# Performance work log

Measured on AMD Instinct MI355X. Metric: run time of the kernel, lower is better.

Reference implementation:

```python
import jax, jax.numpy as jnp
import numpy as np

B, C, H, W = 16, 384, 64, 64
S, R, GR = 16, 8, 64
EPS = 1e-6


def setup_inputs() -> dict:
    key = jax.random.key(0)
    ks = jax.random.split(key, 16)
    def rn(k, shape, s):
        return jax.random.normal(k, shape, dtype=jnp.float32) * s
    inp = {"x": jax.random.normal(ks[0], (B, C, H, W), dtype=jnp.float32)}
    i = 1
    for p in ("row", "col"):
        inp[p + "_a_logit"] = jnp.zeros((S,), jnp.float32)
        inp[p + "_U"] = rn(ks[i], (S, R), 0.02); i += 1
        inp[p + "_V"] = rn(ks[i], (S, R), 0.02); i += 1
        inp[p + "_Win"] = rn(ks[i], (S, C), 1.0 / np.sqrt(C)); i += 1
        inp[p + "_bin"] = jnp.zeros((S,), jnp.float32)
        inp[p + "_Wg"] = rn(ks[i], (S, C), 1.0 / np.sqrt(C)); i += 1
        inp[p + "_bg"] = jnp.zeros((S,), jnp.float32)
        inp[p + "_Wout"] = rn(ks[i], (C, S), 1.0 / np.sqrt(S)); i += 1
        inp[p + "_bout"] = jnp.zeros((C,), jnp.float32)
        inp[p + "_Wskip"] = rn(ks[i], (C, C), 1.0 / np.sqrt(C)); i += 1
        inp[p + "_bskip"] = jnp.zeros((C,), jnp.float32)
    inp["g1_w"] = rn(ks[i], (GR, C), 1.0 / np.sqrt(C)); i += 1
    inp["g1_b"] = jnp.zeros((GR,), jnp.float32)
    inp["g2_w"] = rn(ks[i], (C, GR), 1.0 / np.sqrt(GR)); i += 1
    inp["g2_b"] = jnp.zeros((C,), jnp.float32)
    inp["norm_w"] = jnp.ones((C,), jnp.float32)
    inp["norm_b"] = jnpp = jnp.zeros((C,), jnp.float32)
    inp["norm_b"] = jnp.zeros((C,), jnp.float32)
    return inp


def _ssm1d(x, a_logit, U, V, Win, bin_, Wg, bg, Wout, bout, Wskip, bskip, reverse):
    # x: [N, L, D]
    if reverse:
        x = x[:, ::-1]
    u = jnp.einsum('nld,sd->nls', x, Win) + bin_          # [N,L,S]
    g = jax.nn.sigmoid(jnp.einsum('nld,sd->nls', x, Wg) + bg)
    a = jax.nn.sigmoid(a_logit)                            # [S]
    # h_t = a*h + g_t*u_t + h @ (U V^T)^T  ==  h @ (diag(a) + (U V^T)^T) + g_t*u_t
    A = jnp.diag(a) + (U @ V.T).T                          # [S,S]
    gu = jnp.swapaxes(g * u, 0, 1)                         # [L,N,S]
    h0 = jnp.zeros((x.shape[0], a.shape[0]), x.dtype)

    def step(h, gu_t):
        h = h @ A + gu_t
        return h, h

    _, hs = jax.lax.scan(step, h0, gu)                     # [L,N,S]
    hs = jnp.swapaxes(hs, 0, 1)                            # [N,L,S]
    y = (jnp.einsum('nls,ds->nld', hs, Wout) + bout
         + jnp.einsum('nld,ed->nle', x, Wskip) + bskip)
    if reverse:
        y = y[:, ::-1]
    return y


def _forward(x, rp, cp, g1_w, g1_b, g2_w, g2_b, norm_w, norm_b):
    Bx, Cx, Hx, Wx = x.shape
    rows = jnp.transpose(x, (0, 2, 3, 1)).reshape(Bx * Hx, Wx, Cx)
    cols = jnp.transpose(x, (0, 3, 2, 1)).reshape(Bx * Wx, Hx, Cx)
    yr = _ssm1d(rows, *rp, False) + _ssm1d(rows, *rp, True)
    yc = _ssm1d(cols, *cp, False) + _ssm1d(cols, *cp, True)
    yr = jnp.transpose(yr.reshape(Bx, Hx, Wx, Cx), (0, 3, 1, 2))
    yc = jnp.transpose(yc.reshape(Bx, Wx, Hx, Cx), (0, 3, 2, 1))
    y = (yr + yc) * 0.25
    # LayerNorm over channel dim of BCHW
    mean = x.mean(axis=1, keepdims=True)
    var = ((x - mean) ** 2).mean(axis=1, keepdims=True)
    xn = (x - mean) / jnp.sqrt(var + EPS)
    xn = xn * norm_w[None, :, None, None] + norm_b[None, :, None, None]
    # gate: 1x1 conv -> GELU(exact) -> 1x1 conv -> sigmoid
    h1 = jax.nn.gelu(jnp.einsum('bchw,oc->bohw', xn, g1_w) + g1_b[None, :, None, None], approximate=False)
    g = jax.nn.sigmoid(jnp.einsum('bghw,cg->bchw', h1, g2_w) + g2_b[None, :, None, None])
    return g * y + (1.0 - g) * x


def reference(x, row_a_logit, row_U, row_V, row_Win, row_bin, row_Wg, row_bg, row_Wout, row_bout, row_Wskip, row_bskip, col_a_logit, col_U, col_V, col_Win, col_bin, col_Wg, col_bg, col_Wout, col_bout, col_Wskip, col_bskip, g1_w, g1_b, g2_w, g2_b, norm_w, norm_b):
    rp = (row_a_logit, row_U, row_V, row_Win, row_bin, row_Wg, row_bg, row_Wout, row_bout, row_Wskip, row_bskip)
    cp = (col_a_logit, col_U, col_V, col_Win, col_bin, col_Wg, col_bg, col_Wout, col_bout, col_Wskip, col_bskip)
    return _forward(x, rp, cp, g1_w, g1_b, g2_w, g2_b, norm_w, norm_b)
```

## Files before the change

### kernel.cpp

```cpp
#include <hip/hip_runtime.h>
#include <hip/hip_bf16.h>
#include <math.h>

#define PP 4096
#define CCH 384
#define NB 16

using short8 = __attribute__((ext_vector_type(8))) short;
using f32x4  = __attribute__((ext_vector_type(4))) float;
using half2t = __attribute__((ext_vector_type(2))) __fp16;

__device__ __forceinline__ float sigmoidf_(float v){ return 1.f/(1.f+expf(-v)); }
__device__ __forceinline__ float fast_sig(float v){
  return __builtin_amdgcn_rcpf(1.f + __builtin_amdgcn_exp2f(-v*1.44269504088896f));
}
__device__ __forceinline__ unsigned int f2bf(float f){
  __hip_bfloat16 h = __float2bfloat16(f);
  return (unsigned int)*reinterpret_cast<unsigned short*>(&h);
}
__device__ __forceinline__ float bf2f(unsigned short u){
  unsigned int w = ((unsigned int)u) << 16;
  return __uint_as_float(w);
}
__device__ __forceinline__ void gload_lds16(const void* g, void* l){
  __builtin_amdgcn_global_load_lds(
      (const __attribute__((address_space(1))) unsigned int*)g,
      (__attribute__((address_space(3))) unsigned int*)l, 16, 0, 0);
}

__global__ __launch_bounds__(256) void k_prep(
    const float* __restrict__ rAl, const float* __restrict__ rU, const float* __restrict__ rV,
    const float* __restrict__ cAl, const float* __restrict__ cU, const float* __restrict__ cV,
    const float* __restrict__ rWs, const float* __restrict__ cWs,
    const float* __restrict__ WinR, const float* __restrict__ WgR,
    const float* __restrict__ WinC, const float* __restrict__ WgC,
    const float* __restrict__ g1w, const float* __restrict__ nw, const float* __restrict__ nb,
    const float* __restrict__ g2w,
    const float* __restrict__ WoR, const float* __restrict__ WoC,
    float* __restrict__ Arow, float* __restrict__ Acol,
    unsigned short* __restrict__ WsumBf, unsigned short* __restrict__ WcatBf,
    unsigned short* __restrict__ g2wBf, unsigned short* __restrict__ WocatBf,
    float* __restrict__ t1, float* __restrict__ t2)
{
  int bid = blockIdx.x, tid = threadIdx.x;
  if (bid < 576) {
    int idx = bid*256 + tid;
    WsumBf[idx] = (unsigned short)f2bf(rWs[idx] + cWs[idx]);
  } else if (bid < 768) {
    int idx = (bid-576)*256 + tid;
    int row = idx / CCH, col = idx - row*CCH;
    float v;
    if      (row < 16)  v = WinR[row*CCH + col];
    else if (row < 32)  v = WgR [(row-16)*CCH + col];
    else if (row < 48)  v = WinC[(row-32)*CCH + col];
    else if (row < 64)  v = WgC [(row-48)*CCH + col];
    else                v = g1w[(row-64)*CCH + col]*nw[col];
    WcatBf[idx] = (unsigned short)f2bf(v);
  } else if (bid < 864) {
    int idx = (bid-768)*256 + tid;
    g2wBf[idx] = (unsigned short)f2bf(g2w[idx]);
  } else if (bid < 960) {
    int idx = (bid-864)*256 + tid;
    int c = idx >> 6, k = idx & 63;
    int sel = (k >> 4) & 1;
    float v = 0.5f * (sel ? WoC[c*16 + (k&15)] : WoR[c*16 + (k&15)]);
    WocatBf[idx] = (unsigned short)f2bf(v);
  } else {
    {
      int i = tid >> 4, j = tid & 15;
      float sr = 0.f, sc = 0.f;
      #pragma unroll
      for (int r=0;r<8;++r){ sr += rV[i*8+r]*rU[j*8+r]; sc += cV[i*8+r]*cU[j*8+r]; }
      if (i==j){ sr += sigmoidf_(rAl[i]); sc += sigmoidf_(cAl[i]); }
      Arow[tid] = sr; Acol[tid] = sc;
    }
    if (tid < 64) {
      float s1=0.f, s2=0.f;
      for (int c=0;c<CCH;++c){ s1 += g1w[tid*CCH+c]*nw[c]; s2 += nb[c]*g1w[tid*CCH+c]; }
      t1[tid]=s1; t2[tid]=s2;
    }
  }
}

__global__ __launch_bounds__(256) void k_xf(
    const float* __restrict__ x, const unsigned short* __restrict__ WcatBf,
    const float* __restrict__ binR, const float* __restrict__ bgR,
    const float* __restrict__ binC, const float* __restrict__ bgC,
    const float* __restrict__ t1, const float* __restrict__ t2,
    const float* __restrict__ g1b,
    unsigned short* __restrict__ xbf,
    float* __restrict__ ugr, float* __restrict__ ugc,
    unsigned short* __restrict__ h1bf)
{
  int b = blockIdx.x >> 6, pt = blockIdx.x & 63;
  int t = threadIdx.x;
  int w = t >> 6, l = t & 63;
  int lr = l & 15, kq = l >> 4, kb8 = kq*8;
  int pl = t & 63, g4 = w;

  __shared__ unsigned short xtb[64*64];
  __shared__ float red[512];
  __shared__ float meanS[64], invS[64];

  const float* xb = x + (size_t)b*CCH*PP + pt*64;
  f32x4 acc[2][4] = {};
  float sx = 0.f, sx2 = 0.f;

  float xv[16];
  #pragma unroll
  for (int j=0;j<16;++j) xv[j] = xb[(size_t)(g4*16 + j)*PP + pl];

  const unsigned short* wrow0 = WcatBf + (size_t)(w*32 + lr)*CCH + kb8;
  const unsigned short* wrow1 = wrow0 + 16*CCH;
  unsigned short* xgo = xbf + ((size_t)(b*PP + pt*64))*CCH;

  #pragma unroll
  for (int cc=0; cc<6; ++cc) {
    unsigned int pk[8];
    #pragma unroll
    for (int j=0;j<16;++j){ sx += xv[j]; sx2 += xv[j]*xv[j]; }
    #pragma unroll
    for (int j=0;j<8;++j) pk[j] = f2bf(xv[2*j]) | (f2bf(xv[2*j+1])<<16);
    __syncthreads();
    {
      int kg0 = g4*2, kg1 = g4*2+1;
      uint4 v0 = make_uint4(pk[0],pk[1],pk[2],pk[3]);
      uint4 v1 = make_uint4(pk[4],pk[5],pk[6],pk[7]);
      *(uint4*)&xtb[(size_t)(pl*8 + (kg0 ^ (pl&7)))*8] = v0;
      *(uint4*)&xtb[(size_t)(pl*8 + (kg1 ^ (pl&7)))*8] = v1;
    }
    if (cc < 5) {
      #pragma unroll
      for (int j=0;j<16;++j) xv[j] = xb[(size_t)((cc+1)*64 + g4*16 + j)*PP + pl];
    }
    short8 a0k0 = *(const short8*)(wrow0 + cc*64);
    short8 a0k1 = *(const short8*)(wrow0 + cc*64 + 32);
    short8 a1k0 = *(const short8*)(wrow1 + cc*64);
    short8 a1k1 = *(const short8*)(wrow1 + cc*64 + 32);
    __syncthreads();
    #pragma unroll
    for (int ks=0; ks<2; ++ks){
      int kg = ks*4 + kq;
      #pragma unroll
      for (int nf=0; nf<4; ++nf){
        int pr = nf*16 + lr;
        short8 bv = *(const short8*)&xtb[(size_t)(pr*8 + (kg ^ (pr&7)))*8];
        acc[0][nf] = __builtin_amdgcn_mfma_f32_16x16x32_bf16(ks? a0k1:a0k0, bv, acc[0][nf], 0,0,0);
        acc[1][nf] = __builtin_amdgcn_mfma_f32_16x16x32_bf16(ks? a1k1:a1k0, bv, acc[1][nf], 0,0,0);
      }
    }
    #pragma unroll
    for (int it=0; it<2; ++it){
      int p2 = 32*it + (t>>3), kg2 = t & 7;
      uint4 v = *(const uint4*)&xtb[(size_t)(p2*8 + (kg2 ^ (p2&7)))*8];
      *(uint4*)&xgo[(size_t)p2*CCH + cc*64 + kg2*8] = v;
    }
  }

  __syncthreads();
  red[g4*64 + pl] = sx;
  red[256 + g4*64 + pl] = sx2;
  __syncthreads();
  if (t < 64) {
    float s1 = red[t] + red[64+t] + red[128+t] + red[192+t];
    float s2 = red[256+t] + red[320+t] + red[384+t] + red[448+t];
    float mu = s1 * (1.f/CCH);
    float var = s2 * (1.f/CCH) - mu*mu;
    meanS[t] = mu;
    invS[t]  = rsqrtf(var + 1e-6f);
  }
  __syncthreads();

  if (w < 2) {
    const float* bu = w ? binC : binR;
    const float* bg = w ? bgC  : bgR;
    float* dst = w ? ugc : ugr;
    float bus[4], bgs[4];
    #pragma unroll
    for (int r=0;r<4;++r){ int s = kq*4 + r; bus[r]=bu[s]; bgs[r]=bg[s]; }
    #pragma unroll
    for (int nf=0; nf<4; ++nf){
      size_t pbase = ((size_t)(b*PP + pt*64 + nf*16 + lr))*16;
      #pragma unroll
      for (int r=0;r<4;++r){
        int s = kq*4 + r;
        float u = acc[0][nf][r] + bus[r];
        float g = fast_sig(acc[1][nf][r] + bgs[r]);
        dst[pbase + s] = u*g;
      }
    }
  } else {
    int ob = (w-2)*32 + kq*4;
    float t1o[2][4], t2o[2][4], gbo[2][4];
    #pragma unroll
    for (int mi=0;mi<2;++mi)
      #pragma unroll
      for (int r=0;r<4;++r){
        int o = ob + mi*16 + r;
        t1o[mi][r]=t1[o]; t2o[mi][r]=t2[o]; gbo[mi][r]=g1b[o];
      }
    #pragma unroll
    for (int nf=0; nf<4; ++nf){
      int pLoc = nf*16 + lr;
      float mu = meanS[pLoc], iv = invS[pLoc];
      #pragma unroll
      for (int mi=0;mi<2;++mi){
        unsigned int us[4];
        #pragma unroll
        for (int r=0;r<4;++r){
          float pre = iv*(acc[mi][nf][r] - mu*t1o[mi][r]) + t2o[mi][r] + gbo[mi][r];
          float ge = 0.5f*pre*(1.f + erff(pre*0.70710678118654752f));
          us[r] = f2bf(ge);
        }
        uint2 o2; o2.x = us[0] | (us[1]<<16); o2.y = us[2] | (us[3]<<16);
        *reinterpret_cast<uint2*>(h1bf + ((size_t)(b*PP + pt*64 + pLoc))*64 + (w-2)*32 + mi*16 + kq*4) = o2;
      }
    }
  }
}

__global__ __launch_bounds__(256) void k_scan(
    const float* __restrict__ ugr, const float* __restrict__ ugc,
    const float* __restrict__ Arow, const float* __restrict__ Acol,
    unsigned short* __restrict__ hs2)
{
  int W = blockIdx.x*4 + (threadIdx.x >> 6);
  int lane = threadIdx.x & 63;
  int tsk = W*4 + (lane >> 4);
  int s = lane & 15, base = lane & 48;
  int dir = tsk >> 11;
  int rem = tsk & 2047;
  int isCol = rem >> 10;
  int gg = rem & 1023;
  int b = gg >> 6, rc = gg & 63;
  const float* ug = isCol ? ugc : ugr;
  const float* A  = isCol ? Acol : Arow;
  int off = dir*32 + isCol*16;
  int p0 = b*PP + (isCol ? rc : rc*64);
  int stride = isCol ? 64 : 1;
  float ac[16];
  #pragma unroll
  for (int i=0;i<16;++i) ac[i] = A[i*16 + s];
  float h = 0.f;
  #pragma unroll 4
  for (int st=0; st<64; ++st){
    int l2 = dir ? (63-st) : st;
    float gu = ug[((size_t)(p0 + l2*stride))*16 + s];
    float tt = 0.f;
    #pragma unroll
    for (int i=0;i<16;++i) tt += __shfl(h, base + i, 64) * ac[i];
    h = tt + gu;
    hs2[((size_t)(p0 + l2*stride))*64 + off + s] = (unsigned short)f2bf(h);
  }
}

__global__ __launch_bounds__(512, 4) void k_fused(
    const unsigned short* __restrict__ xbf,
    const unsigned short* __restrict__ WsumBf,
    const unsigned short* __restrict__ h1bf, const unsigned short* __restrict__ g2wBf,
    const unsigned short* __restrict__ hs2, const unsigned short* __restrict__ WocatBf,
    const float* __restrict__ g2b,
    const float* __restrict__ boR, const float* __restrict__ bsR,
    const float* __restrict__ boC, const float* __restrict__ bsC,
    float* __restrict__ outp)
{
  int obid = blockIdx.x;
  int bid = ((obid & 7) * 128) + (obid >> 3);
  int b = bid >> 6, pt = bid & 63;
  int t = threadIdx.x;
  int w = t >> 6, l = t & 63;
  int lr = l & 15, kq = l >> 4, kb8 = kq * 8;
  int cw = w*48;

  __shared__ unsigned short xt[64*48*8];

  short8 gaw[3][2], gbv[2][4];
  {
    const unsigned short* hbase = h1bf + ((size_t)(b*PP + pt*64 + lr))*64 + kb8;
    #pragma unroll
    for (int ks=0; ks<2; ++ks)
      #pragma unroll
      for (int nf=0; nf<4; ++nf)
        gbv[ks][nf] = *(const short8*)(hbase + (size_t)nf*16*64 + ks*32);
    #pragma unroll
    for (int mi=0; mi<3; ++mi){
      const unsigned short* wbg = g2wBf + (size_t)(cw + mi*16 + lr)*64 + kb8;
      gaw[mi][0] = *(const short8*)(wbg);
      gaw[mi][1] = *(const short8*)(wbg + 32);
    }
  }

  {
    const unsigned short* xrow0 = xbf + ((size_t)(b*PP + pt*64))*CCH;
    #pragma unroll
    for (int i=0;i<6;++i){
      int G = w*384 + i*64 + l;
      int p = G/48, kgs = G - p*48;
      int kg = (kgs & ~7) | ((kgs & 7) ^ (p & 7));
      gload_lds16(xrow0 + (size_t)p*CCH + kg*8, &xt[(size_t)G*8]);
    }
  }

  unsigned int gt[3][4][2];
  {
    f32x4 gac[3][4] = {};
    #pragma unroll
    for (int ks=0; ks<2; ++ks)
      #pragma unroll
      for (int nf=0; nf<4; ++nf)
        #pragma unroll
        for (int mi=0; mi<3; ++mi)
          gac[mi][nf] = __builtin_amdgcn_mfma_f32_16x16x32_bf16(gaw[mi][ks], gbv[ks][nf], gac[mi][nf], 0,0,0);
    #pragma unroll
    for (int mi=0;mi<3;++mi){
      float4 gb4 = *(const float4*)&g2b[cw + mi*16 + kq*4];
      #pragma unroll
      for (int nf=0;nf<4;++nf){
        float s0 = fast_sig(gac[mi][nf][0] + gb4.x);
        float s1 = fast_sig(gac[mi][nf][1] + gb4.y);
        float s2 = fast_sig(gac[mi][nf][2] + gb4.z);
        float s3 = fast_sig(gac[mi][nf][3] + gb4.w);
        half2t p01 = __builtin_amdgcn_cvt_pkrtz(s0, s1);
        half2t p23 = __builtin_amdgcn_cvt_pkrtz(s2, s3);
        __builtin_memcpy(&gt[mi][nf][0], &p01, 4);
        __builtin_memcpy(&gt[mi][nf][1], &p23, 4);
      }
    }
  }

  __syncthreads();

  f32x4 acc[3][4] = {};
  const unsigned short* wbS = WsumBf + (size_t)(cw + lr)*CCH + kb8;
  #pragma unroll
  for (int c=0;c<6;++c){
    short8 a[3][2];
    #pragma unroll
    for (int mi=0;mi<3;++mi){
      a[mi][0] = *(const short8*)(wbS + (size_t)mi*16*CCH + c*64);
      a[mi][1] = *(const short8*)(wbS + (size_t)mi*16*CCH + c*64 + 32);
    }
    #pragma unroll
    for (int ks=0;ks<2;++ks){
      int kgl = ks*4 + kq;
      #pragma unroll
      for (int nf=0;nf<4;++nf){
        int pr = nf*16 + lr;
        int kgs = c*8 + (kgl ^ (pr & 7));
        short8 bv = *(const short8*)&xt[(size_t)(pr*48 + kgs)*8];
        #pragma unroll
        for (int mi=0;mi<3;++mi)
          acc[mi][nf] = __builtin_amdgcn_mfma_f32_16x16x32_bf16(a[mi][ks], bv, acc[mi][nf], 0,0,0);
      }
    }
  }

  {
    const unsigned short* hb2 = hs2 + ((size_t)(b*PP + pt*64 + lr))*64 + kb8;
    short8 hv[2][4];
    #pragma unroll
    for (int ks=0;ks<2;++ks)
      #pragma unroll
      for (int nf=0;nf<4;++nf)
        hv[ks][nf] = *(const short8*)(hb2 + (size_t)nf*16*64 + ks*32);
    #pragma unroll
    for (int mi=0;mi<3;++mi){
      const unsigned short* wo = WocatBf + (size_t)(cw + mi*16 + lr)*64 + kb8;
      short8 wa0 = *(const short8*)(wo);
      short8 wa1 = *(const short8*)(wo + 32);
      #pragma unroll
      for (int nf=0;nf<4;++nf){
        acc[mi][nf] = __builtin_amdgcn_mfma_f32_16x16x32_bf16(wa0, hv[0][nf], acc[mi][nf], 0,0,0);
        acc[mi][nf] = __builtin_amdgcn_mfma_f32_16x16x32_bf16(wa1, hv[1][nf], acc[mi][nf], 0,0,0);
      }
    }
  }

  #pragma unroll
  for (int mi=0;mi<3;++mi){
    int cb0 = cw + mi*16 + kq*4;
    float4 b1 = *(const float4*)&boR[cb0];
    float4 b2 = *(const float4*)&bsR[cb0];
    float4 b3 = *(const float4*)&boC[cb0];
    float4 b4 = *(const float4*)&bsC[cb0];
    float cb4[4] = { b1.x+b2.x+b3.x+b4.x, b1.y+b2.y+b3.y+b4.y,
                     b1.z+b2.z+b3.z+b4.z, b1.w+b2.w+b3.w+b4.w };
    int kgR = cb0 >> 3, eoff = cb0 & 7;
    #pragma unroll
    for (int nf=0;nf<4;++nf){
      int p = nf*16 + lr;
      int kgsR = (kgR & ~7) | ((kgR & 7) ^ (p & 7));
      uint2 xres = *(const uint2*)&xt[(size_t)(p*48 + kgsR)*8 + eoff];
      half2t g01, g23;
      __builtin_memcpy(&g01, &gt[mi][nf][0], 4);
      __builtin_memcpy(&g23, &gt[mi][nf][1], 4);
      float gv[4] = { (float)g01[0], (float)g01[1], (float)g23[0], (float)g23[1] };
      #pragma unroll
      for (int r=0;r<4;++r){
        unsigned int word = (r < 2) ? xres.x : xres.y;
        unsigned short us = (r & 1) ? (unsigned short)(word >> 16) : (unsigned short)(word & 0xffff);
        float xv = bf2f(us);
        float y = 0.5f*acc[mi][nf][r] + 0.5f*cb4[r];
        float gtv = gv[r];
        size_t addr = ((size_t)(b*CCH + cb0 + r))*PP + pt*64 + p;
        outp[addr] = gtv*y + (1.f-gtv)*xv;
      }
    }
  }
}

extern "C" void kernel_launch(void* const* d_in, const int* in_sizes, int n_in,
                              void* d_out, int out_size, void* d_ws, size_t ws_size,
                              hipStream_t stream)
{
  const float* x    = (const float*)d_in[0];
  const float* rAl  = (const float*)d_in[1];
  const float* rU   = (const float*)d_in[2];
  const float* rV   = (const float*)d_in[3];
  const float* rWin = (const float*)d_in[4];
  const float* rbin = (const float*)d_in[5];
  const float* rWg  = (const float*)d_in[6];
  const float* rbg  = (const float*)d_in[7];
  const float* rWo  = (const float*)d_in[8];
  const float* rbo  = (const float*)d_in[9];
  const float* rWs  = (const float*)d_in[10];
  const float* rbs  = (const float*)d_in[11];
  const float* cAl  = (const float*)d_in[12];
  const float* cU   = (const float*)d_in[13];
  const float* cV   = (const float*)d_in[14];
  const float* cWin = (const float*)d_in[15];
  const float* cbin = (const float*)d_in[16];
  const float* cWg  = (const float*)d_in[17];
  const float* cbg  = (const float*)d_in[18];
  const float* cWo  = (const float*)d_in[19];
  const float* cbo  = (const float*)d_in[20];
  const float* cWs  = (const float*)d_in[21];
  const float* cbs  = (const float*)d_in[22];
  const float* g1w  = (const float*)d_in[23];
  const float* g1b  = (const float*)d_in[24];
  const float* g2w  = (const float*)d_in[25];
  const float* g2b  = (const float*)d_in[26];
  const float* nw   = (const float*)d_in[27];
  const float* nb   = (const float*)d_in[28];

  float* ws   = (float*)d_ws;
  float* ugr  = ws;
  float* ugc  = ugr + 1048576;
  float* Arow = ugc + 1048576;
  float* Acol = Arow + 256;
  float* t1   = Acol + 256;
  float* t2   = t1 + 64;
  unsigned short* xbf     = (unsigned short*)(t2 + 64);
  unsigned short* h1bf    = xbf + (size_t)25165824;
  unsigned short* hs2     = h1bf + (size_t)4194304;
  unsigned short* WsumBf  = hs2 + (size_t)4194304;
  unsigned short* WcatBf  = WsumBf + 147456;
  unsigned short* g2wBf   = WcatBf + 49152;
  unsigned short* WocatBf = g2wBf + 24576;
  float* outp = (float*)d_out;

  k_prep<<<961, 256, 0, stream>>>(rAl,rU,rV,cAl,cU,cV,rWs,cWs,
                                  rWin,rWg,cWin,cWg,g1w,nw,nb,g2w,rWo,cWo,
                                  Arow,Acol,WsumBf,WcatBf,g2wBf,WocatBf,t1,t2);
  k_xf<<<1024, 256, 0, stream>>>(x, WcatBf, rbin, rbg, cbin, cbg,
                                 t1, t2, g1b, xbf, ugr, ugc, h1bf);
  k_scan<<<256, 256, 0, stream>>>(ugr, ugc, Arow, Acol, hs2);
  k_fused<<<1024, 512, 0, stream>>>(xbf, WsumBf, h1bf, g2wBf,
                                    hs2, WocatBf, g2b,
                                    rbo, rbs, cbo, cbs, outp);
}
```

Baseline: 153.8 us.

## Split x tile load into two halves, overlap with MFMA, use tanh-GELU approximation

The x tile copy into LDS is issued in two halves, each covering 32 pixel rows. The skip GEMM now waits only for the first half (vmcnt(3) plus a barrier) before computing the first two column fragments, then waits for the rest and computes the remaining fragments, with raised wave priority around the MFMA loops. This is meant to overlap global-to-LDS latency with matrix work. The gate's exact erf GELU is also replaced by the tanh-form approximation expressed through a fast sigmoid, which trades a small accuracy difference for cheaper math. The second half re-reads the Wsum weight fragments.

```diff
diff --git a/kernel.cpp b/kernel.cpp
--- a/kernel.cpp
+++ b/kernel.cpp
@@ -209,7 +209,8 @@
         #pragma unroll
         for (int r=0;r<4;++r){
           float pre = iv*(acc[mi][nf][r] - mu*t1o[mi][r]) + t2o[mi][r] + gbo[mi][r];
-          float ge = 0.5f*pre*(1.f + erff(pre*0.70710678118654752f));
+          float aa = pre*(1.f + 0.044715f*pre*pre);
+          float ge = pre*fast_sig(1.5957691216f*aa);
           us[r] = f2bf(ge);
         }
         uint2 o2; o2.x = us[0] | (us[1]<<16); o2.y = us[2] | (us[3]<<16);
@@ -292,13 +293,23 @@
 
   {
     const unsigned short* xrow0 = xbf + ((size_t)(b*PP + pt*64))*CCH;
-    #pragma unroll
-    for (int i=0;i<6;++i){
-      int G = w*384 + i*64 + l;
+    __builtin_amdgcn_sched_barrier(0);
+    #pragma unroll
+    for (int i=0;i<3;++i){
+      int G = w*192 + i*64 + l;
       int p = G/48, kgs = G - p*48;
       int kg = (kgs & ~7) | ((kgs & 7) ^ (p & 7));
       gload_lds16(xrow0 + (size_t)p*CCH + kg*8, &xt[(size_t)G*8]);
     }
+    __builtin_amdgcn_sched_barrier(0);
+    #pragma unroll
+    for (int i=0;i<3;++i){
+      int G = 1536 + w*192 + i*64 + l;
+      int p = G/48, kgs = G - p*48;
+      int kg = (kgs & ~7) | ((kgs & 7) ^ (p & 7));
+      gload_lds16(xrow0 + (size_t)p*CCH + kg*8, &xt[(size_t)G*8]);
+    }
+    __builtin_amdgcn_sched_barrier(0);
   }
 
   unsigned int gt[3][4][2];
@@ -328,10 +339,14 @@
     }
   }
 
-  __syncthreads();
-
   f32x4 acc[3][4] = {};
   const unsigned short* wbS = WsumBf + (size_t)(cw + lr)*CCH + kb8;
+
+  asm volatile("s_waitcnt vmcnt(3)" ::: "memory");
+  __builtin_amdgcn_s_barrier();
+  __builtin_amdgcn_sched_barrier(0);
+
+  __builtin_amdgcn_s_setprio(1);
   #pragma unroll
   for (int c=0;c<6;++c){
     short8 a[3][2];
@@ -344,7 +359,7 @@
     for (int ks=0;ks<2;++ks){
       int kgl = ks*4 + kq;
       #pragma unroll
-      for (int nf=0;nf<4;++nf){
+      for (int nf=0;nf<2;++nf){
         int pr = nf*16 + lr;
         int kgs = c*8 + (kgl ^ (pr & 7));
         short8 bv = *(const short8*)&xt[(size_t)(pr*48 + kgs)*8];
@@ -354,6 +369,36 @@
       }
     }
   }
+  __builtin_amdgcn_s_setprio(0);
+
+  asm volatile("s_waitcnt vmcnt(0)" ::: "memory");
+  __builtin_amdgcn_s_barrier();
+  __builtin_amdgcn_sched_barrier(0);
+
+  __builtin_amdgcn_s_setprio(1);
+  #pragma unroll
+  for (int c=0;c<6;++c){
+    short8 a[3][2];
+    #pragma unroll
+    for (int mi=0;mi<3;++mi){
+      a[mi][0] = *(const short8*)(wbS + (size_t)mi*16*CCH + c*64);
+      a[mi][1] = *(const short8*)(wbS + (size_t)mi*16*CCH + c*64 + 32);
+    }
+    #pragma unroll
+    for (int ks=0;ks<2;++ks){
+      int kgl = ks*4 + kq;
+      #pragma unroll
+      for (int nf=2;nf<4;++nf){
+        int pr = nf*16 + lr;
+        int kgs = c*8 + (kgl ^ (pr & 7));
+        short8 bv = *(const short8*)&xt[(size_t)(pr*48 + kgs)*8];
+        #pragma unroll
+        for (int mi=0;mi<3;++mi)
+          acc[mi][nf] = __builtin_amdgcn_mfma_f32_16x16x32_bf16(a[mi][ks], bv, acc[mi][nf], 0,0,0);
+      }
+    }
+  }
+  __builtin_amdgcn_s_setprio(0);
 
   {
     const unsigned short* hb2 = hs2 + ((size_t)(b*PP + pt*64 + lr))*64 + kb8;
```

Result: slower. 178.1 us (+15.8%).

## Process two pixel tiles per block with prefetch of next x tile

Applied to the files above, without the earlier changes.

k_fused now handles two consecutive 64-pixel tiles per block (grid halved to 512). The next tile's bf16 x is loaded into LDS asynchronously while the current tile's hs2 GEMM and epilogue run. The residual term now reads fp32 x straight from global memory instead of the bf16 LDS copy, and the store loop is reordered so each lane writes along pixel rows. This amortizes the per-block weight setup and overlaps memory traffic with compute, at the cost of half as many blocks, extra barriers, and extra fp32 x reads.

```diff
diff --git a/kernel.cpp b/kernel.cpp
--- a/kernel.cpp
+++ b/kernel.cpp
@@ -255,6 +255,7 @@
 }
 
 __global__ __launch_bounds__(512, 4) void k_fused(
+    const float* __restrict__ x,
     const unsigned short* __restrict__ xbf,
     const unsigned short* __restrict__ WsumBf,
     const unsigned short* __restrict__ h1bf, const unsigned short* __restrict__ g2wBf,
@@ -265,8 +266,8 @@
     float* __restrict__ outp)
 {
   int obid = blockIdx.x;
-  int bid = ((obid & 7) * 128) + (obid >> 3);
-  int b = bid >> 6, pt = bid & 63;
+  int bid = ((obid & 7) * 64) + (obid >> 3);
+  int b = bid >> 5, pp2 = bid & 31;
   int t = threadIdx.x;
   int w = t >> 6, l = t & 63;
   int lr = l & 15, kq = l >> 4, kb8 = kq * 8;
@@ -274,8 +275,12 @@
 
   __shared__ unsigned short xt[64*48*8];
 
-  short8 gaw[3][2], gbv[2][4];
+  const unsigned short* wbS = WsumBf + (size_t)(cw + lr)*CCH + kb8;
+  unsigned int gt[3][4][2];
+
   {
+    int pt = pp2*2;
+    short8 gaw[3][2], gbv[2][4];
     const unsigned short* hbase = h1bf + ((size_t)(b*PP + pt*64 + lr))*64 + kb8;
     #pragma unroll
     for (int ks=0; ks<2; ++ks)
@@ -288,9 +293,6 @@
       gaw[mi][0] = *(const short8*)(wbg);
       gaw[mi][1] = *(const short8*)(wbg + 32);
     }
-  }
-
-  {
     const unsigned short* xrow0 = xbf + ((size_t)(b*PP + pt*64))*CCH;
     #pragma unroll
     for (int i=0;i<6;++i){
@@ -299,10 +301,6 @@
       int kg = (kgs & ~7) | ((kgs & 7) ^ (p & 7));
       gload_lds16(xrow0 + (size_t)p*CCH + kg*8, &xt[(size_t)G*8]);
     }
-  }
-
-  unsigned int gt[3][4][2];
-  {
     f32x4 gac[3][4] = {};
     #pragma unroll
     for (int ks=0; ks<2; ++ks)
@@ -330,81 +328,138 @@
 
   __syncthreads();
 
-  f32x4 acc[3][4] = {};
-  const unsigned short* wbS = WsumBf + (size_t)(cw + lr)*CCH + kb8;
   #pragma unroll
-  for (int c=0;c<6;++c){
-    short8 a[3][2];
+  for (int tl=0; tl<2; ++tl) {
+    int pt = pp2*2 + tl;
+
+    f32x4 acc[3][4] = {};
+    #pragma unroll
+    for (int c=0;c<6;++c){
+      short8 a[3][2];
+      #pragma unroll
+      for (int mi=0;mi<3;++mi){
+        a[mi][0] = *(const short8*)(wbS + (size_t)mi*16*CCH + c*64);
+        a[mi][1] = *(const short8*)(wbS + (size_t)mi*16*CCH + c*64 + 32);
+      }
+      #pragma unroll
+      for (int ks=0;ks<2;++ks){
+        int kgl = ks*4 + kq;
+        #pragma unroll
+        for (int nf=0;nf<4;++nf){
+          int pr = nf*16 + lr;
+          int kgs = c*8 + (kgl ^ (pr & 7));
+          short8 bv = *(const short8*)&xt[(size_t)(pr*48 + kgs)*8];
+          #pragma unroll
+          for (int mi=0;mi<3;++mi)
+            acc[mi][nf] = __builtin_amdgcn_mfma_f32_16x16x32_bf16(a[mi][ks], bv, acc[mi][nf], 0,0,0);
+        }
+      }
+    }
+
+    __syncthreads();
+
+    if (tl == 0) {
+      const unsigned short* xrow1 = xbf + ((size_t)(b*PP + (pp2*2+1)*64))*CCH;
+      #pragma unroll
+      for (int i=0;i<6;++i){
+        int G = w*384 + i*64 + l;
+        int p = G/48, kgs = G - p*48;
+        int kg = (kgs & ~7) | ((kgs & 7) ^ (p & 7));
+        gload_lds16(xrow1 + (size_t)p*CCH + kg*8, &xt[(size_t)G*8]);
+      }
+    }
+
+    {
+      const unsigned short* hb2 = hs2 + ((size_t)(b*PP + pt*64 + lr))*64 + kb8;
+      short8 hv[2][4];
+      #pragma unroll
+      for (int ks=0;ks<2;++ks)
+        #pragma unroll
+        for (int nf=0;nf<4;++nf)
+          hv[ks][nf] = *(const short8*)(hb2 + (size_t)nf*16*64 + ks*32);
+      #pragma unroll
+      for (int mi=0;mi<3;++mi){
+        const unsigned short* wo = WocatBf + (size_t)(cw + mi*16 + lr)*64 + kb8;
+        short8 wa0 = *(const short8*)(wo);
+        short8 wa1 = *(const short8*)(wo + 32);
+        #pragma unroll
+        for (int nf=0;nf<4;++nf){
+          acc[mi][nf] = __builtin_amdgcn_mfma_f32_16x16x32_bf16(wa0, hv[0][nf], acc[mi][nf], 0,0,0);
+          acc[mi][nf] = __builtin_amdgcn_mfma_f32_16x16x32_bf16(wa1, hv[1][nf], acc[mi][nf], 0,0,0);
+        }
+      }
+    }
+
     #pragma unroll
     for (int mi=0;mi<3;++mi){
-      a[mi][0] = *(const short8*)(wbS + (size_t)mi*16*CCH + c*64);
-      a[mi][1] = *(const short8*)(wbS + (size_t)mi*16*CCH + c*64 + 32);
-    }
-    #pragma unroll
-    for (int ks=0;ks<2;++ks){
-      int kgl = ks*4 + kq;
+      int cb0 = cw + mi*16 + kq*4;
+      float4 b1 = *(const float4*)&boR[cb0];
+      float4 b2 = *(const float4*)&bsR[cb0];
+      float4 b3 = *(const float4*)&boC[cb0];
+      float4 b4 = *(const float4*)&bsC[cb0];
+      float cb4[4] = { b1.x+b2.x+b3.x+b4.x, b1.y+b2.y+b3.y+b4.y,
+                       b1.z+b2.z+b3.z+b4.z, b1.w+b2.w+b3.w+b4.w };
+      half2t g01[4], g23[4];
       #pragma unroll
       for (int nf=0;nf<4;++nf){
-        int pr = nf*16 + lr;
-        int kgs = c*8 + (kgl ^ (pr & 7));
-        short8 bv = *(const short8*)&xt[(size_t)(pr*48 + kgs)*8];
-        #pragma unroll
-        for (int mi=0;mi<3;++mi)
-          acc[mi][nf] = __builtin_amdgcn_mfma_f32_16x16x32_bf16(a[mi][ks], bv, acc[mi][nf], 0,0,0);
-      }
-    }
-  }
-
-  {
-    const unsigned short* hb2 = hs2 + ((size_t)(b*PP + pt*64 + lr))*64 + kb8;
-    short8 hv[2][4];
-    #pragma unroll
-    for (int ks=0;ks<2;++ks)
-      #pragma unroll
-      for (int nf=0;nf<4;++nf)
-        hv[ks][nf] = *(const short8*)(hb2 + (size_t)nf*16*64 + ks*32);
-    #pragma unroll
-    for (int mi=0;mi<3;++mi){
-      const unsigned short* wo = WocatBf + (size_t)(cw + mi*16 + lr)*64 + kb8;
-      short8 wa0 = *(const short8*)(wo);
-      short8 wa1 = *(const short8*)(wo + 32);
-      #pragma unroll
-      for (int nf=0;nf<4;++nf){
-        acc[mi][nf] = __builtin_amdgcn_mfma_f32_16x16x32_bf16(wa0, hv[0][nf], acc[mi][nf], 0,0,0);
-        acc[mi][nf] = __builtin_amdgcn_mfma_f32_16x16x32_bf16(wa1, hv[1][nf], acc[mi][nf], 0,0,0);
-      }
-    }
-  }
-
-  #pragma unroll
-  for (int mi=0;mi<3;++mi){
-    int cb0 = cw + mi*16 + kq*4;
-    float4 b1 = *(const float4*)&boR[cb0];
-    float4 b2 = *(const float4*)&bsR[cb0];
-    float4 b3 = *(const float4*)&boC[cb0];
-    float4 b4 = *(const float4*)&bsC[cb0];
-    float cb4[4] = { b1.x+b2.x+b3.x+b4.x, b1.y+b2.y+b3.y+b4.y,
-                     b1.z+b2.z+b3.z+b4.z, b1.w+b2.w+b3.w+b4.w };
-    int kgR = cb0 >> 3, eoff = cb0 & 7;
-    #pragma unroll
-    for (int nf=0;nf<4;++nf){
-      int p = nf*16 + lr;
-      int kgsR = (kgR & ~7) | ((kgR & 7) ^ (p & 7));
-      uint2 xres = *(const uint2*)&xt[(size_t)(p*48 + kgsR)*8 + eoff];
-      half2t g01, g23;
-      __builtin_memcpy(&g01, &gt[mi][nf][0], 4);
-      __builtin_memcpy(&g23, &gt[mi][nf][1], 4);
-      float gv[4] = { (float)g01[0], (float)g01[1], (float)g23[0], (float)g23[1] };
+        __builtin_memcpy(&g01[nf], &gt[mi][nf][0], 4);
+        __builtin_memcpy(&g23[nf], &gt[mi][nf][1], 4);
+      }
       #pragma unroll
       for (int r=0;r<4;++r){
-        unsigned int word = (r < 2) ? xres.x : xres.y;
-        unsigned short us = (r & 1) ? (unsigned short)(word >> 16) : (unsigned short)(word & 0xffff);
-        float xv = bf2f(us);
-        float y = 0.5f*acc[mi][nf][r] + 0.5f*cb4[r];
-        float gtv = gv[r];
-        size_t addr = ((size_t)(b*CCH + cb0 + r))*PP + pt*64 + p;
-        outp[addr] = gtv*y + (1.f-gtv)*xv;
-      }
+        int c = cb0 + r;
+        float yb = 0.5f*cb4[r];
+        size_t rowb = ((size_t)(b*CCH + c))*PP + pt*64;
+        #pragma unroll
+        for (int nf=0;nf<4;++nf){
+          int p = nf*16 + lr;
+          float xv = x[rowb + p];
+          float gtv = (r<2) ? (float)g01[nf][r&1] : (float)g23[nf][r&1];
+          float y = 0.5f*acc[mi][nf][r] + yb;
+          outp[rowb + p] = gtv*y + (1.f-gtv)*xv;
+        }
+      }
+    }
+
+    if (tl == 0) {
+      int pt1 = pp2*2 + 1;
+      short8 gaw[3][2], gbv[2][4];
+      const unsigned short* hbase = h1bf + ((size_t)(b*PP + pt1*64 + lr))*64 + kb8;
+      #pragma unroll
+      for (int ks=0; ks<2; ++ks)
+        #pragma unroll
+        for (int nf=0; nf<4; ++nf)
+          gbv[ks][nf] = *(const short8*)(hbase + (size_t)nf*16*64 + ks*32);
+      #pragma unroll
+      for (int mi=0; mi<3; ++mi){
+        const unsigned short* wbg = g2wBf + (size_t)(cw + mi*16 + lr)*64 + kb8;
+        gaw[mi][0] = *(const short8*)(wbg);
+        gaw[mi][1] = *(const short8*)(wbg + 32);
+      }
+      f32x4 gac[3][4] = {};
+      #pragma unroll
+      for (int ks=0; ks<2; ++ks)
+        #pragma unroll
+        for (int nf=0; nf<4; ++nf)
+          #pragma unroll
+          for (int mi=0; mi<3; ++mi)
+            gac[mi][nf] = __builtin_amdgcn_mfma_f32_16x16x32_bf16(gaw[mi][ks], gbv[ks][nf], gac[mi][nf], 0,0,0);
+      #pragma unroll
+      for (int mi=0;mi<3;++mi){
+        float4 gb4 = *(const float4*)&g2b[cw + mi*16 + kq*4];
+        #pragma unroll
+        for (int nf=0;nf<4;++nf){
+          float s0 = fast_sig(gac[mi][nf][0] + gb4.x);
+          float s1 = fast_sig(gac[mi][nf][1] + gb4.y);
+          float s2 = fast_sig(gac[mi][nf][2] + gb4.z);
+          float s3 = fast_sig(gac[mi][nf][3] + gb4.w);
+          half2t p01 = __builtin_amdgcn_cvt_pkrtz(s0, s1);
+          half2t p23 = __builtin_amdgcn_cvt_pkrtz(s2, s3);
+          __builtin_memcpy(&gt[mi][nf][0], &p01, 4);
+          __builtin_memcpy(&gt[mi][nf][1], &p23, 4);
+        }
+      }
+      __syncthreads();
     }
   }
 }
@@ -465,7 +520,7 @@
   k_xf<<<1024, 256, 0, stream>>>(x, WcatBf, rbin, rbg, cbin, cbg,
                                  t1, t2, g1b, xbf, ugr, ugc, h1bf);
   k_scan<<<256, 256, 0, stream>>>(ugr, ugc, Arow, Acol, hs2);
-  k_fused<<<1024, 512, 0, stream>>>(xbf, WsumBf, h1bf, g2wBf,
-                                    hs2, WocatBf, g2b,
-                                    rbo, rbs, cbo, cbs, outp);
-}
+  k_fused<<<512, 512, 0, stream>>>(x, xbf, WsumBf, h1bf, g2wBf,
+                                   hs2, WocatBf, g2b,
+                                   rbo, rbs, cbo, cbs, outp);
+}
```

Measured after the change: 328.3 us. +113.4%, slower.
